# Kernel tuning notes

Hardware: AMD Instinct MI355X
Metric: run time of the kernel (lower is better)

## Reference

```python
import jax, jax.numpy as jnp
import numpy as np

EPS = 1e-8
DIGIT_TEMPERATURE = 1.0
SEED = 0
B, KMAX, V = 64, 16, 32000
DV, H = 10, 4096
# permute_prob table: prob_table[k] = permute_prob.get(k, 0.0)
_PROB = np.zeros(KMAX + 1, dtype=np.float32)
_PROB[2:] = 0.5
PROB_TABLE = jnp.asarray(_PROB)


def setup_inputs() -> dict:
    key = jax.random.key(0)
    ks = jax.random.split(key, 6)
    p_raw = jax.random.uniform(ks[0], (B, KMAX, V), dtype=jnp.float32)
    p_z = p_raw / p_raw.sum(axis=-1, keepdims=True)  # valid distributions per slot
    return {
        "p_z": p_z,
        "digit_logits_ref": jax.random.normal(ks[1], (B, DV), dtype=jnp.float32),
        "digit_logits_cf": jax.random.normal(ks[2], (B, DV), dtype=jnp.float32),
        "h_ans_ref": jax.random.normal(ks[3], (B, H), dtype=jnp.float32),
        "h_ans_cf": jax.random.normal(ks[4], (B, H), dtype=jnp.float32),
        "k_vals": jax.random.randint(ks[5], (B,), 0, KMAX + 1),
    }


def _js_divergence(p, q, eps=EPS):
    p = jnp.clip(p.astype(jnp.float32), eps)
    q = jnp.clip(q.astype(jnp.float32), eps)
    m = 0.5 * (p + q)
    log_m = jnp.log(m)
    kl_pm = (p * (jnp.log(p) - log_m)).sum(-1)
    kl_qm = (q * (jnp.log(q) - log_m)).sum(-1)
    return 0.5 * (kl_pm + kl_qm)


def _build_counterfactual_pz(p_z, k_vals):
    # Vectorized GS-mode counterfactual: per batch, with prob permute_prob[k]
    # (and k>1) permute the first k slots, otherwise temperature-warp them.
    bsz, kmax, vocab = p_z.shape
    key = jax.random.key(SEED)
    k_dec, k_perm, k_tau = jax.random.split(key, 3)
    u_dec = jax.random.uniform(k_dec, (bsz,))
    do_permute = (k_vals > 1) & (u_dec < PROB_TABLE[k_vals])  # [B]
    slots = jnp.arange(kmax)
    active = slots[None, :] < k_vals[:, None]  # [B, K]
    # ragged permutation of the first k slots: argsort random keys, inactive -> +inf
    u_perm = jax.random.uniform(k_perm, (bsz, kmax))
    perm = jnp.argsort(jnp.where(active, u_perm, jnp.inf), axis=1)  # stable: tail keeps order
    permuted = jnp.take_along_axis(p_z, perm[:, :, None], axis=1)
    # temperature warp: softmax(log(p)/tau), tau ~ U(0.7, 1.6) per slot
    tau = jax.random.uniform(k_tau, (bsz, kmax, 1), minval=0.7, maxval=1.6)
    warped = jax.nn.softmax(jnp.log(jnp.clip(p_z, EPS)) / tau, axis=-1)
    cf = jnp.where(do_permute[:, None, None], permuted, warped)
    return jnp.where(active[:, :, None], cf, p_z)


def reference(p_z, digit_logits_ref, digit_logits_cf, h_ans_ref, h_ans_cf, k_vals):
    p_cf_z = _build_counterfactual_pz(p_z, k_vals)
    # safe_softmax(logits, tau) == softmax(logits / tau)
    p_ref = jax.lax.stop_gradient(
        jax.nn.softmax(digit_logits_ref / DIGIT_TEMPERATURE, axis=-1))
    p_cf = jax.nn.softmax(digit_logits_cf / DIGIT_TEMPERATURE, axis=-1)
    js = _js_divergence(p_ref, p_cf).mean()
    loss_cf = jnp.log(jnp.float32(2.0)) - js
    ref_f = jax.lax.stop_gradient(h_ans_ref.astype(jnp.float32))
    cf_f = h_ans_cf.astype(jnp.float32)
    ref_norm = ref_f / jnp.clip(jnp.linalg.norm(ref_f, axis=-1, keepdims=True), 1e-12)
    cf_norm = cf_f / jnp.clip(jnp.linalg.norm(cf_f, axis=-1, keepdims=True), 1e-12)
    cos_sim = (ref_norm * cf_norm).sum(-1).mean()
    loss_dep = cos_sim - 1.0  # cf_mode == 'gs'
    dep_norm = jnp.linalg.norm(ref_f - cf_f, axis=-1).mean()
    return loss_cf, loss_dep, dep_norm, p_cf_z
```

## Files before the change

kernel.cpp:

```cpp
#include <hip/hip_runtime.h>
#include <stdint.h>

#define NB    64
#define KMAX  16
#define VV    32000
#define DVV   10
#define HH    4096
#define NROWS (NB*KMAX)
#define EPSF  1e-8f
#define NQ    8000

__device__ __forceinline__ uint32_t rotl32(uint32_t v, int r) { return (v << r) | (v >> (32 - r)); }

__device__ __forceinline__ void tf2x32(uint32_t k0, uint32_t k1, uint32_t c0, uint32_t c1,
                                       uint32_t& o0, uint32_t& o1) {
    uint32_t ks2 = k0 ^ k1 ^ 0x1BD11BDAu;
    uint32_t x0 = c0 + k0, x1 = c1 + k1;
    const int RA[4] = {13, 15, 26, 6};
    const int RB[4] = {17, 29, 16, 24};
#pragma unroll
    for (int i = 0; i < 4; ++i) { x0 += x1; x1 = rotl32(x1, RA[i]); x1 ^= x0; }
    x0 += k1; x1 += ks2 + 1u;
#pragma unroll
    for (int i = 0; i < 4; ++i) { x0 += x1; x1 = rotl32(x1, RB[i]); x1 ^= x0; }
    x0 += ks2; x1 += k0 + 2u;
#pragma unroll
    for (int i = 0; i < 4; ++i) { x0 += x1; x1 = rotl32(x1, RA[i]); x1 ^= x0; }
    x0 += k0; x1 += k1 + 3u;
#pragma unroll
    for (int i = 0; i < 4; ++i) { x0 += x1; x1 = rotl32(x1, RB[i]); x1 ^= x0; }
    x0 += k1; x1 += ks2 + 4u;
#pragma unroll
    for (int i = 0; i < 4; ++i) { x0 += x1; x1 = rotl32(x1, RA[i]); x1 ^= x0; }
    x0 += ks2; x1 += k0 + 5u;
    o0 = x0; o1 = x1;
}

__device__ __forceinline__ float bits_to_u01(uint32_t bits) {
    uint32_t fb = (bits >> 9) | 0x3F800000u;
    return __uint_as_float(fb) - 1.0f;
}

__global__ __launch_bounds__(1024) void cf_main_kernel(const float* __restrict__ p_z,
                                                       const int* __restrict__ k_vals,
                                                       float* __restrict__ out) {
    const int row = blockIdx.x;
    const int b = row >> 4, s = row & 15;
    const int tid = threadIdx.x;
    float* dst = out + (size_t)row * VV;

    __shared__ int   s_src;
    __shared__ float s_itau;

    if (tid < 16) {
        const int t = tid;
        uint32_t a0, b0_, a1, b1_, a2, b2_, y0, y1;
        tf2x32(0u, 0u, 0u, 3u, a0, b0_);
        tf2x32(0u, 0u, 1u, 4u, a1, b1_);
        tf2x32(0u, 0u, 2u, 5u, a2, b2_);
        const uint32_t kdec0 = a0, kdec1 = a1;
        const uint32_t kperm0 = a2, kperm1 = b0_;
        const uint32_t ktau0 = b1_, ktau1 = b2_;

        const int k = k_vals[b];

        uint32_t bits;
        if (b < 32) { tf2x32(kdec0, kdec1, (uint32_t)b, (uint32_t)(b + 32), y0, y1); bits = y0; }
        else        { tf2x32(kdec0, kdec1, (uint32_t)(b - 32), (uint32_t)b, y0, y1); bits = y1; }
        const float u_dec = bits_to_u01(bits);
        const bool dp = (k > 1) && (u_dec < ((k >= 2) ? 0.5f : 0.0f));

        const int j = (b << 4) + t;
        uint32_t pb;
        if (j < 512) { tf2x32(kperm0, kperm1, (uint32_t)j, (uint32_t)(j + 512), y0, y1); pb = y0; }
        else         { tf2x32(kperm0, kperm1, (uint32_t)(j - 512), (uint32_t)j, y0, y1); pb = y1; }
        const float up = bits_to_u01(pb);

        const float INF = __int_as_float(0x7F800000);
        const float keyt = (t < k) ? up : INF;
        int r = 0;
#pragma unroll
        for (int tt = 0; tt < KMAX; ++tt) {
            float kt = __shfl(keyt, tt, 64);
            r += (kt < keyt) || (kt == keyt && tt < t);
        }

        if (s >= k)  { if (t == 0) { s_src = s; s_itau = 0.f; } }
        else if (dp) { if (r == s) { s_src = t; s_itau = 0.f; } }
        else if (t == 0) {
            const int js = (b << 4) + s;
            uint32_t tb;
            if (js < 512) { tf2x32(ktau0, ktau1, (uint32_t)js, (uint32_t)(js + 512), y0, y1); tb = y0; }
            else          { tf2x32(ktau0, ktau1, (uint32_t)(js - 512), (uint32_t)js, y0, y1); tb = y1; }
            const float tau = fmaxf(0.7f, bits_to_u01(tb) * 0.9f + 0.7f);
            s_src = -1; s_itau = 1.0f / tau;
        }
    }
    __syncthreads();

    const int src = s_src;

    if (src >= 0) {
        const float* sp = p_z + ((size_t)((b << 4) + src)) * VV;
#pragma unroll
        for (int i = 0; i < 8; ++i) {
            const int q = tid + (i << 10);
            if (q < NQ - 1) {
                float4 v = *(const float4*)(sp + (q << 2) + 1);
                *(float4*)(dst + (q << 2) + 1) = v;
            }
        }
        if (tid == 0) dst[0] = sp[0];
        if (tid == 1) {
            dst[VV - 3] = sp[VV - 3];
            dst[VV - 2] = sp[VV - 2];
            dst[VV - 1] = sp[VV - 1];
        }
        return;
    }

    const float it = s_itau;
    const float* sp = p_z + (size_t)row * VV;
    float4 r[8];
    float e0 = 0.f, t0 = 0.f, t1 = 0.f, t2 = 0.f;
    float lsum = 0.f;
#pragma unroll
    for (int i = 0; i < 8; ++i) {
        const int q = tid + (i << 10);
        if (q < NQ - 1) {
            float4 v = *(const float4*)(sp + (q << 2) + 1);
            v.x = exp2f(__log2f(fmaxf(v.x, EPSF)) * it);
            v.y = exp2f(__log2f(fmaxf(v.y, EPSF)) * it);
            v.z = exp2f(__log2f(fmaxf(v.z, EPSF)) * it);
            v.w = exp2f(__log2f(fmaxf(v.w, EPSF)) * it);
            r[i] = v;
            lsum += v.x + v.y + v.z + v.w;
        } else {
            r[i] = make_float4(0.f, 0.f, 0.f, 0.f);
        }
    }
    if (tid == 0) { e0 = exp2f(__log2f(fmaxf(sp[0], EPSF)) * it); lsum += e0; }
    if (tid == 1) {
        t0 = exp2f(__log2f(fmaxf(sp[VV - 3], EPSF)) * it);
        t1 = exp2f(__log2f(fmaxf(sp[VV - 2], EPSF)) * it);
        t2 = exp2f(__log2f(fmaxf(sp[VV - 1], EPSF)) * it);
        lsum += t0 + t1 + t2;
    }
    __shared__ float red[16];
    float t = lsum;
#pragma unroll
    for (int o = 32; o; o >>= 1) t += __shfl_down(t, o, 64);
    if ((tid & 63) == 0) red[tid >> 6] = t;
    __syncthreads();
    if (tid < 64) {
        float u = (tid < 16) ? red[tid] : 0.0f;
#pragma unroll
        for (int o = 8; o; o >>= 1) u += __shfl_down(u, o, 64);
        if (tid == 0) red[0] = u;
    }
    __syncthreads();
    const float scale = 1.0f / red[0];

#pragma unroll
    for (int i = 0; i < 8; ++i) {
        const int q = tid + (i << 10);
        if (q < NQ - 1) {
            float4 st;
            st.x = r[i].x * scale; st.y = r[i].y * scale;
            st.z = r[i].z * scale; st.w = r[i].w * scale;
            *(float4*)(dst + (q << 2) + 1) = st;
        }
    }
    if (tid == 0) dst[0] = e0 * scale;
    if (tid == 1) {
        dst[VV - 3] = t0 * scale;
        dst[VV - 2] = t1 * scale;
        dst[VV - 1] = t2 * scale;
    }
}

__global__ __launch_bounds__(256) void rowred_kernel(const float* __restrict__ hr,
                                                     const float* __restrict__ hc,
                                                     float* __restrict__ cosb,
                                                     float* __restrict__ depb) {
    int b = blockIdx.x;
    const float4* r4 = (const float4*)(hr + (size_t)b * HH);
    const float4* c4 = (const float4*)(hc + (size_t)b * HH);
    float srr = 0.f, scc = 0.f, sxc = 0.f, sdd = 0.f;
    for (int i = threadIdx.x; i < HH / 4; i += 256) {
        float4 r = r4[i], c = c4[i];
        srr += r.x * r.x + r.y * r.y + r.z * r.z + r.w * r.w;
        scc += c.x * c.x + c.y * c.y + c.z * c.z + c.w * c.w;
        sxc += r.x * c.x + r.y * c.y + r.z * c.z + r.w * c.w;
        float dx = r.x - c.x, dy = r.y - c.y, dz = r.z - c.z, dw = r.w - c.w;
        sdd += dx * dx + dy * dy + dz * dz + dw * dw;
    }
#pragma unroll
    for (int o = 32; o; o >>= 1) {
        srr += __shfl_down(srr, o, 64);
        scc += __shfl_down(scc, o, 64);
        sxc += __shfl_down(sxc, o, 64);
        sdd += __shfl_down(sdd, o, 64);
    }
    __shared__ float red[4][4];
    int w = threadIdx.x >> 6;
    if ((threadIdx.x & 63) == 0) { red[w][0] = srr; red[w][1] = scc; red[w][2] = sxc; red[w][3] = sdd; }
    __syncthreads();
    if (threadIdx.x == 0) {
        float t0 = 0.f, t1 = 0.f, t2 = 0.f, t3 = 0.f;
        for (int i = 0; i < 4; ++i) { t0 += red[i][0]; t1 += red[i][1]; t2 += red[i][2]; t3 += red[i][3]; }
        float nr = fmaxf(sqrtf(t0), 1e-12f);
        float nc = fmaxf(sqrtf(t1), 1e-12f);
        cosb[b] = t2 / (nr * nc);
        depb[b] = sqrtf(t3);
    }
}

__global__ void finalize_kernel(const float* __restrict__ dlr, const float* __restrict__ dlc,
                                const float* __restrict__ cosb, const float* __restrict__ depb,
                                float* __restrict__ out) {
    int b = threadIdx.x;
    float lr[DVV], lc[DVV];
    float mr = -1e30f, mc = -1e30f;
#pragma unroll
    for (int v = 0; v < DVV; ++v) {
        lr[v] = dlr[b * DVV + v]; lc[v] = dlc[b * DVV + v];
        mr = fmaxf(mr, lr[v]); mc = fmaxf(mc, lc[v]);
    }
    float sr = 0.f, sc = 0.f;
#pragma unroll
    for (int v = 0; v < DVV; ++v) {
        lr[v] = expf(lr[v] - mr); sr += lr[v];
        lc[v] = expf(lc[v] - mc); sc += lc[v];
    }
    float js = 0.f;
#pragma unroll
    for (int v = 0; v < DVV; ++v) {
        float p = fmaxf(lr[v] / sr, EPSF);
        float q = fmaxf(lc[v] / sc, EPSF);
        float m = 0.5f * (p + q);
        float lm = logf(m);
        js += 0.5f * (p * (logf(p) - lm) + q * (logf(q) - lm));
    }
    float cs = cosb[b], dp = depb[b];
#pragma unroll
    for (int o = 32; o; o >>= 1) {
        js += __shfl_down(js, o, 64);
        cs += __shfl_down(cs, o, 64);
        dp += __shfl_down(dp, o, 64);
    }
    if (b == 0) {
        out[0] = logf(2.0f) - js * (1.0f / 64.0f);
        out[1] = cs * (1.0f / 64.0f) - 1.0f;
        out[2] = dp * (1.0f / 64.0f);
    }
}

extern "C" void kernel_launch(void* const* d_in, const int* in_sizes, int n_in,
                              void* d_out, int out_size, void* d_ws, size_t ws_size,
                              hipStream_t stream) {
    const float* p_z = (const float*)d_in[0];
    const float* dlr = (const float*)d_in[1];
    const float* dlc = (const float*)d_in[2];
    const float* hr  = (const float*)d_in[3];
    const float* hc  = (const float*)d_in[4];
    const int*   kv  = (const int*)d_in[5];
    float* out = (float*)d_out;

    float* cosb = (float*)d_ws;
    float* depb = cosb + NB;

    cf_main_kernel<<<NROWS, 1024, 0, stream>>>(p_z, kv, out + 3);
    rowred_kernel<<<NB, 256, 0, stream>>>(hr, hc, cosb, depb);
    finalize_kernel<<<1, 64, 0, stream>>>(dlr, dlc, cosb, depb, out);
}
```

Measured before the change: 57.97 us.

## Fuse three kernels into one mega-kernel with atomic last-block finalize and nontemporal stores

```diff
diff --git a/kernel.cpp b/kernel.cpp
--- a/kernel.cpp
+++ b/kernel.cpp
@@ -10,6 +10,8 @@
 #define EPSF  1e-8f
 #define NQ    8000
 
+typedef float floatx4 __attribute__((ext_vector_type(4)));
+
 __device__ __forceinline__ uint32_t rotl32(uint32_t v, int r) { return (v << r) | (v >> (32 - r)); }
 
 __device__ __forceinline__ void tf2x32(uint32_t k0, uint32_t k1, uint32_t c0, uint32_t c1,
@@ -41,13 +43,102 @@
     return __uint_as_float(fb) - 1.0f;
 }
 
-__global__ __launch_bounds__(1024) void cf_main_kernel(const float* __restrict__ p_z,
-                                                       const int* __restrict__ k_vals,
-                                                       float* __restrict__ out) {
-    const int row = blockIdx.x;
+__device__ __forceinline__ void nt_store4(float* p, float a, float b, float c, float d) {
+    floatx4 v = {a, b, c, d};
+    __builtin_nontemporal_store(v, (floatx4*)p);
+}
+
+__global__ __launch_bounds__(1024) void mega_kernel(const float* __restrict__ p_z,
+                                                    const int* __restrict__ k_vals,
+                                                    const float* __restrict__ dlr,
+                                                    const float* __restrict__ dlc,
+                                                    const float* __restrict__ hr,
+                                                    const float* __restrict__ hc,
+                                                    float* __restrict__ cosb,
+                                                    float* __restrict__ depb,
+                                                    int* __restrict__ counter,
+                                                    float* __restrict__ out) {
+    const int tid = threadIdx.x;
+
+    if (blockIdx.x < NB) {
+        const int b = blockIdx.x;
+        const float4* r4 = (const float4*)(hr + (size_t)b * HH);
+        const float4* c4 = (const float4*)(hc + (size_t)b * HH);
+        float4 rr = r4[tid], cc = c4[tid];
+        float srr = rr.x * rr.x + rr.y * rr.y + rr.z * rr.z + rr.w * rr.w;
+        float scc = cc.x * cc.x + cc.y * cc.y + cc.z * cc.z + cc.w * cc.w;
+        float sxc = rr.x * cc.x + rr.y * cc.y + rr.z * cc.z + rr.w * cc.w;
+        float dx = rr.x - cc.x, dy = rr.y - cc.y, dz = rr.z - cc.z, dw = rr.w - cc.w;
+        float sdd = dx * dx + dy * dy + dz * dz + dw * dw;
+#pragma unroll
+        for (int o = 32; o; o >>= 1) {
+            srr += __shfl_down(srr, o, 64);
+            scc += __shfl_down(scc, o, 64);
+            sxc += __shfl_down(sxc, o, 64);
+            sdd += __shfl_down(sdd, o, 64);
+        }
+        __shared__ float red[16][4];
+        __shared__ int s_ticket;
+        const int w = tid >> 6;
+        if ((tid & 63) == 0) { red[w][0] = srr; red[w][1] = scc; red[w][2] = sxc; red[w][3] = sdd; }
+        __syncthreads();
+        if (tid == 0) {
+            float t0 = 0.f, t1 = 0.f, t2 = 0.f, t3 = 0.f;
+            for (int i = 0; i < 16; ++i) { t0 += red[i][0]; t1 += red[i][1]; t2 += red[i][2]; t3 += red[i][3]; }
+            float nr = fmaxf(sqrtf(t0), 1e-12f);
+            float nc = fmaxf(sqrtf(t1), 1e-12f);
+            cosb[b] = t2 / (nr * nc);
+            depb[b] = sqrtf(t3);
+            __threadfence();
+            s_ticket = atomicAdd(counter, 1);
+        }
+        __syncthreads();
+        if (s_ticket != NB - 1) return;
+        __threadfence();
+
+        if (tid < 64) {
+            const int bb = tid;
+            float lr[DVV], lc[DVV];
+            float mr = -1e30f, mc = -1e30f;
+#pragma unroll
+            for (int v = 0; v < DVV; ++v) {
+                lr[v] = dlr[bb * DVV + v]; lc[v] = dlc[bb * DVV + v];
+                mr = fmaxf(mr, lr[v]); mc = fmaxf(mc, lc[v]);
+            }
+            float sr = 0.f, sc = 0.f;
+#pragma unroll
+            for (int v = 0; v < DVV; ++v) {
+                lr[v] = expf(lr[v] - mr); sr += lr[v];
+                lc[v] = expf(lc[v] - mc); sc += lc[v];
+            }
+            float js = 0.f;
+#pragma unroll
+            for (int v = 0; v < DVV; ++v) {
+                float p = fmaxf(lr[v] / sr, EPSF);
+                float q = fmaxf(lc[v] / sc, EPSF);
+                float m = 0.5f * (p + q);
+                float lm = logf(m);
+                js += 0.5f * (p * (logf(p) - lm) + q * (logf(q) - lm));
+            }
+            float cs = cosb[bb], dpv = depb[bb];
+#pragma unroll
+            for (int o = 32; o; o >>= 1) {
+                js += __shfl_down(js, o, 64);
+                cs += __shfl_down(cs, o, 64);
+                dpv += __shfl_down(dpv, o, 64);
+            }
+            if (tid == 0) {
+                out[0] = logf(2.0f) - js * (1.0f / 64.0f);
+                out[1] = cs * (1.0f / 64.0f) - 1.0f;
+                out[2] = dpv * (1.0f / 64.0f);
+            }
+        }
+        return;
+    }
+
+    const int row = blockIdx.x - NB;
     const int b = row >> 4, s = row & 15;
-    const int tid = threadIdx.x;
-    float* dst = out + (size_t)row * VV;
+    float* dst = out + 3 + (size_t)row * VV;
 
     __shared__ int   s_src;
     __shared__ float s_itau;
@@ -107,7 +198,7 @@
             const int q = tid + (i << 10);
             if (q < NQ - 1) {
                 float4 v = *(const float4*)(sp + (q << 2) + 1);
-                *(float4*)(dst + (q << 2) + 1) = v;
+                nt_store4(dst + (q << 2) + 1, v.x, v.y, v.z, v.w);
             }
         }
         if (tid == 0) dst[0] = sp[0];
@@ -146,29 +237,27 @@
         t2 = exp2f(__log2f(fmaxf(sp[VV - 1], EPSF)) * it);
         lsum += t0 + t1 + t2;
     }
-    __shared__ float red[16];
+    __shared__ float red1[16];
     float t = lsum;
 #pragma unroll
     for (int o = 32; o; o >>= 1) t += __shfl_down(t, o, 64);
-    if ((tid & 63) == 0) red[tid >> 6] = t;
+    if ((tid & 63) == 0) red1[tid >> 6] = t;
     __syncthreads();
     if (tid < 64) {
-        float u = (tid < 16) ? red[tid] : 0.0f;
+        float u = (tid < 16) ? red1[tid] : 0.0f;
 #pragma unroll
         for (int o = 8; o; o >>= 1) u += __shfl_down(u, o, 64);
-        if (tid == 0) red[0] = u;
+        if (tid == 0) red1[0] = u;
     }
     __syncthreads();
-    const float scale = 1.0f / red[0];
+    const float scale = 1.0f / red1[0];
 
 #pragma unroll
     for (int i = 0; i < 8; ++i) {
         const int q = tid + (i << 10);
         if (q < NQ - 1) {
-            float4 st;
-            st.x = r[i].x * scale; st.y = r[i].y * scale;
-            st.z = r[i].z * scale; st.w = r[i].w * scale;
-            *(float4*)(dst + (q << 2) + 1) = st;
+            nt_store4(dst + (q << 2) + 1,
+                      r[i].x * scale, r[i].y * scale, r[i].z * scale, r[i].w * scale);
         }
     }
     if (tid == 0) dst[0] = e0 * scale;
@@ -176,83 +265,6 @@
         dst[VV - 3] = t0 * scale;
         dst[VV - 2] = t1 * scale;
         dst[VV - 1] = t2 * scale;
-    }
-}
-
-__global__ __launch_bounds__(256) void rowred_kernel(const float* __restrict__ hr,
-                                                     const float* __restrict__ hc,
-                                                     float* __restrict__ cosb,
-                                                     float* __restrict__ depb) {
-    int b = blockIdx.x;
-    const float4* r4 = (const float4*)(hr + (size_t)b * HH);
-    const float4* c4 = (const float4*)(hc + (size_t)b * HH);
-    float srr = 0.f, scc = 0.f, sxc = 0.f, sdd = 0.f;
-    for (int i = threadIdx.x; i < HH / 4; i += 256) {
-        float4 r = r4[i], c = c4[i];
-        srr += r.x * r.x + r.y * r.y + r.z * r.z + r.w * r.w;
-        scc += c.x * c.x + c.y * c.y + c.z * c.z + c.w * c.w;
-        sxc += r.x * c.x + r.y * c.y + r.z * c.z + r.w * c.w;
-        float dx = r.x - c.x, dy = r.y - c.y, dz = r.z - c.z, dw = r.w - c.w;
-        sdd += dx * dx + dy * dy + dz * dz + dw * dw;
-    }
-#pragma unroll
-    for (int o = 32; o; o >>= 1) {
-        srr += __shfl_down(srr, o, 64);
-        scc += __shfl_down(scc, o, 64);
-        sxc += __shfl_down(sxc, o, 64);
-        sdd += __shfl_down(sdd, o, 64);
-    }
-    __shared__ float red[4][4];
-    int w = threadIdx.x >> 6;
-    if ((threadIdx.x & 63) == 0) { red[w][0] = srr; red[w][1] = scc; red[w][2] = sxc; red[w][3] = sdd; }
-    __syncthreads();
-    if (threadIdx.x == 0) {
-        float t0 = 0.f, t1 = 0.f, t2 = 0.f, t3 = 0.f;
-        for (int i = 0; i < 4; ++i) { t0 += red[i][0]; t1 += red[i][1]; t2 += red[i][2]; t3 += red[i][3]; }
-        float nr = fmaxf(sqrtf(t0), 1e-12f);
-        float nc = fmaxf(sqrtf(t1), 1e-12f);
-        cosb[b] = t2 / (nr * nc);
-        depb[b] = sqrtf(t3);
-    }
-}
-
-__global__ void finalize_kernel(const float* __restrict__ dlr, const float* __restrict__ dlc,
-                                const float* __restrict__ cosb, const float* __restrict__ depb,
-                                float* __restrict__ out) {
-    int b = threadIdx.x;
-    float lr[DVV], lc[DVV];
-    float mr = -1e30f, mc = -1e30f;
-#pragma unroll
-    for (int v = 0; v < DVV; ++v) {
-        lr[v] = dlr[b * DVV + v]; lc[v] = dlc[b * DVV + v];
-        mr = fmaxf(mr, lr[v]); mc = fmaxf(mc, lc[v]);
-    }
-    float sr = 0.f, sc = 0.f;
-#pragma unroll
-    for (int v = 0; v < DVV; ++v) {
-        lr[v] = expf(lr[v] - mr); sr += lr[v];
-        lc[v] = expf(lc[v] - mc); sc += lc[v];
-    }
-    float js = 0.f;
-#pragma unroll
-    for (int v = 0; v < DVV; ++v) {
-        float p = fmaxf(lr[v] / sr, EPSF);
-        float q = fmaxf(lc[v] / sc, EPSF);
-        float m = 0.5f * (p + q);
-        float lm = logf(m);
-        js += 0.5f * (p * (logf(p) - lm) + q * (logf(q) - lm));
-    }
-    float cs = cosb[b], dp = depb[b];
-#pragma unroll
-    for (int o = 32; o; o >>= 1) {
-        js += __shfl_down(js, o, 64);
-        cs += __shfl_down(cs, o, 64);
-        dp += __shfl_down(dp, o, 64);
-    }
-    if (b == 0) {
-        out[0] = logf(2.0f) - js * (1.0f / 64.0f);
-        out[1] = cs * (1.0f / 64.0f) - 1.0f;
-        out[2] = dp * (1.0f / 64.0f);
     }
 }
 
@@ -267,10 +279,11 @@
     const int*   kv  = (const int*)d_in[5];
     float* out = (float*)d_out;
 
-    float* cosb = (float*)d_ws;
-    float* depb = cosb + NB;
-
-    cf_main_kernel<<<NROWS, 1024, 0, stream>>>(p_z, kv, out + 3);
-    rowred_kernel<<<NB, 256, 0, stream>>>(hr, hc, cosb, depb);
-    finalize_kernel<<<1, 64, 0, stream>>>(dlr, dlc, cosb, depb, out);
-}
+    float* cosb    = (float*)d_ws;
+    float* depb    = cosb + NB;
+    int*   counter = (int*)(depb + NB);
+
+    hipMemsetAsync(counter, 0, sizeof(int), stream);
+    mega_kernel<<<NB + NROWS, 1024, 0, stream>>>(p_z, kv, dlr, dlc, hr, hc,
+                                                 cosb, depb, counter, out);
+}
```

Result: slower. 68.53 us (+18.2%).
